# Kernel tuning notes

Hardware: AMD Instinct MI355X
Metric: run time of the kernel (lower is better)

## Reference

```python
import jax, jax.numpy as jnp
import numpy as np

B, T, K, H = 8, 1024, 512, 8
MASKED = True

def setup_inputs() -> dict:
    key = jax.random.key(0)
    ks = jax.random.split(key, 6)
    s = 0.02
    return {
        "x": jax.random.normal(ks[0], (B, T, K), dtype=jnp.float32),
        "Wq": jax.random.normal(ks[1], (K, H * K), dtype=jnp.float32) * s,
        "Wk": jax.random.normal(ks[2], (K, H * K), dtype=jnp.float32) * s,
        "Wv": jax.random.normal(ks[3], (K, H * K), dtype=jnp.float32) * s,
        "Wu": jax.random.normal(ks[4], (H * K, K), dtype=jnp.float32) * s,
        "bu": jnp.zeros((K,), dtype=jnp.float32),
    }

def reference(x, Wq, Wk, Wv, Wu, bu):
    b, t, k = x.shape
    h = H
    scale = k ** (-0.25)  # applied to both q and k, as in the torch module
    q = (x @ Wq).reshape(b, t, h, k) * scale
    kk = (x @ Wk).reshape(b, t, h, k) * scale
    v = (x @ Wv).reshape(b, t, h, k)
    # scores: [b, h, t_q, t_k]
    dot = jnp.einsum("bthk,bshk->bhts", q, kk)
    if MASKED:
        causal = jnp.tril(jnp.ones((t, t), dtype=bool))
        dot = jnp.where(causal, dot, -jnp.inf)
    attn = jax.nn.softmax(dot, axis=-1)
    out = jnp.einsum("bhts,bshk->bthk", attn, v).reshape(b, t, h * k)
    return out @ Wu + bu
```

## Files before the change

kernel.cpp:

```cpp
#include <hip/hip_runtime.h>
#include <hip/hip_bf16.h>

#define T_SEQ 1024
#define NH 8
#define DH 512
#define HK 4096

typedef __attribute__((ext_vector_type(8))) __bf16 bf16x8;
typedef __attribute__((ext_vector_type(4))) float f32x4;

#define QK_SCALE 0.21022410381342863f
#define QK_SCALE_LOG2E 0.30328926584f

static __device__ __forceinline__ unsigned short f2bu(float f) {
  union { __hip_bfloat16 h; unsigned short u; } cv;
  cv.h = __float2bfloat16(f);
  return cv.u;
}

#define GLOAD_LDS16(gsrc, ldst) \
  __builtin_amdgcn_global_load_lds((const __attribute__((address_space(1))) void*)(gsrc), \
                                   (__attribute__((address_space(3))) void*)(ldst), 16, 0, 0)

__global__ void cvt_bf16_kernel(const float* __restrict__ in, unsigned short* __restrict__ out, int n4) {
  int i = blockIdx.x * blockDim.x + threadIdx.x;
  if (i >= n4) return;
  const float4 v = reinterpret_cast<const float4*>(in)[i];
  ushort4 u; u.x = f2bu(v.x); u.y = f2bu(v.y); u.z = f2bu(v.z); u.w = f2bu(v.w);
  reinterpret_cast<ushort4*>(out)[i] = u;
}

__global__ void transpose_cvt_kernel(const float* __restrict__ in, unsigned short* __restrict__ out,
                                     int R, int C) {
  __shared__ float tile[32][33];
  const int c0 = blockIdx.x * 32, r0 = blockIdx.y * 32;
  const int tx = threadIdx.x, ty = threadIdx.y;
  #pragma unroll
  for (int i = ty; i < 32; i += 8)
    tile[i][tx] = in[(size_t)(r0 + i) * C + (c0 + tx)];
  __syncthreads();
  #pragma unroll
  for (int i = ty; i < 32; i += 8)
    out[(size_t)(c0 + i) * R + (r0 + tx)] = f2bu(tile[tx][i]);
}

__global__ void transpose_cvt3_kernel(const float* __restrict__ Wq, const float* __restrict__ Wk,
                                      const float* __restrict__ Wv, unsigned short* __restrict__ out) {
  __shared__ float tile[32][33];
  const float* in = (blockIdx.z == 0) ? Wq : (blockIdx.z == 1) ? Wk : Wv;
  unsigned short* dst = out + (size_t)blockIdx.z * 4096 * 512;
  const int c0 = blockIdx.x * 32, r0 = blockIdx.y * 32;
  const int tx = threadIdx.x, ty = threadIdx.y;
  #pragma unroll
  for (int i = ty; i < 32; i += 8)
    tile[i][tx] = in[(size_t)(r0 + i) * 4096 + (c0 + tx)];
  __syncthreads();
  #pragma unroll
  for (int i = ty; i < 32; i += 8)
    dst[(size_t)(c0 + i) * 512 + (r0 + tx)] = f2bu(tile[tx][i]);
}

__global__ __launch_bounds__(256, 4)
void gemm_qkv(const unsigned short* __restrict__ A,
              const unsigned short* __restrict__ B,
              unsigned short* __restrict__ Qo,
              unsigned short* __restrict__ Ko,
              unsigned short* __restrict__ Vo) {
  __shared__ __align__(16) char smem[32768];
  char* As = smem;
  char* Bs = smem + 16384;
  const int tid = threadIdx.x, lane = tid & 63, w = tid >> 6;
  const int wr = w >> 1, wc = w & 1;
  const int bid = blockIdx.x;
  const int x = bid & 7, inner = bid >> 3;
  const int p0 = (x * 12 + inner % 12) * 128;
  const int p1 = (inner / 12) * 128;
  const int Kd = 512;

  f32x4 acc[4][4];
  #pragma unroll
  for (int i = 0; i < 4; ++i)
    #pragma unroll
    for (int j = 0; j < 4; ++j)
      acc[i][j] = f32x4{0.f, 0.f, 0.f, 0.f};

  for (int kt = 0; kt < Kd; kt += 64) {
    __syncthreads();
    #pragma unroll
    for (int is = 0; is < 4; ++is) {
      const int ob = is * 4096 + w * 1024;
      const int ol = ob + lane * 16;
      const int row = ol >> 7;
      const int bo = ol & 127;
      const int sw = (row & 7) << 4;
      GLOAD_LDS16((const char*)A + ((size_t)(p0 + row) * Kd + kt) * 2 + (bo ^ sw), As + ob);
      GLOAD_LDS16((const char*)B + ((size_t)(p1 + row) * Kd + kt) * 2 + (bo ^ sw), Bs + ob);
    }
    __syncthreads();
    #pragma unroll
    for (int ks = 0; ks < 2; ++ks) {
      bf16x8 af[4], bfr[4];
      #pragma unroll
      for (int mi = 0; mi < 4; ++mi) {
        const int row = wr * 64 + mi * 16 + (lane & 15);
        af[mi] = *reinterpret_cast<const bf16x8*>(
            As + row * 128 + ((ks * 64 + ((lane >> 4) << 4)) ^ ((row & 7) << 4)));
      }
      #pragma unroll
      for (int ni = 0; ni < 4; ++ni) {
        const int row = wc * 64 + ni * 16 + (lane & 15);
        bfr[ni] = *reinterpret_cast<const bf16x8*>(
            Bs + row * 128 + ((ks * 64 + ((lane >> 4) << 4)) ^ ((row & 7) << 4)));
      }
      #pragma unroll
      for (int mi = 0; mi < 4; ++mi)
        #pragma unroll
        for (int ni = 0; ni < 4; ++ni)
          acc[mi][ni] = __builtin_amdgcn_mfma_f32_16x16x32_bf16(af[mi], bfr[ni], acc[mi][ni], 0, 0, 0);
    }
  }

  const int region = p0 >> 12;
  if (region < 2) {
    const float qs = (region == 0) ? QK_SCALE_LOG2E : QK_SCALE;
    unsigned short* dst = (region == 0) ? Qo : Ko;
    #pragma unroll
    for (int mi = 0; mi < 4; ++mi) {
      #pragma unroll
      for (int ni = 0; ni < 4; ++ni) {
        const int n = p0 + wr * 64 + mi * 16 + ((lane >> 4) << 2);
        const int m = p1 + wc * 64 + ni * 16 + (lane & 15);
        const int b = m >> 10, t = m & 1023;
        const int nr = n & 4095, h = nr >> 9, d = nr & 511;
        ushort4 u;
        u.x = f2bu(acc[mi][ni][0] * qs); u.y = f2bu(acc[mi][ni][1] * qs);
        u.z = f2bu(acc[mi][ni][2] * qs); u.w = f2bu(acc[mi][ni][3] * qs);
        *reinterpret_cast<ushort4*>(&dst[((size_t)((b * NH + h) * T_SEQ + t)) * DH + d]) = u;
      }
    }
  } else {
    __syncthreads();
    unsigned short* Vl = reinterpret_cast<unsigned short*>(smem);
    const int key = (lane >> 4) << 3;
    #pragma unroll
    for (int mi = 0; mi < 4; ++mi) {
      #pragma unroll
      for (int ni = 0; ni < 4; ++ni) {
        const int dl = wr * 64 + mi * 16 + ((lane >> 4) << 2);
        const int tl = wc * 64 + ni * 16 + (lane & 15);
        #pragma unroll
        for (int r = 0; r < 4; ++r)
          Vl[(dl + r) * 128 + (tl ^ key)] = f2bu(acc[mi][ni][r]);
      }
    }
    __syncthreads();
    const int bb = p1 >> 10, t0 = p1 & 1023;
    const int hh = (p0 - 8192) >> 9, d0 = p0 & 511;
    unsigned short* vdst = Vo + ((size_t)(bb * NH + hh) * DH + d0) * T_SEQ + t0;
    #pragma unroll
    for (int i = 0; i < 8; ++i) {
      const int idx = i * 256 + tid;
      const int dr = idx >> 4, tc = (idx & 15) * 8;
      const int key2 = ((dr >> 2) & 3) << 3;
      *reinterpret_cast<uint4*>(vdst + (size_t)dr * T_SEQ + tc) =
          *reinterpret_cast<const uint4*>(Vl + dr * 128 + (tc ^ key2));
    }
  }
}

__global__ __launch_bounds__(256, 4)
void gemm_out(const unsigned short* __restrict__ A,
              const unsigned short* __restrict__ B,
              const float* __restrict__ bias,
              float* __restrict__ C) {
  __shared__ __align__(16) char As[8192];
  __shared__ __align__(16) char Bs[16384];
  const int tid = threadIdx.x, lane = tid & 63, w = tid >> 6;
  const int bid = blockIdx.x;
  const int x = bid & 7, inner = bid >> 3;
  const int mtiles_per_xcd = gridDim.x >> 7;
  const int c0 = (inner & 15) * 32;
  const int m0 = (x * mtiles_per_xcd + (inner >> 4)) * 64;
  const int Kd = HK;

  f32x4 acc[2];
  acc[0] = f32x4{0.f, 0.f, 0.f, 0.f};
  acc[1] = f32x4{0.f, 0.f, 0.f, 0.f};

  for (int kt = 0; kt < Kd; kt += 128) {
    __syncthreads();
    #pragma unroll
    for (int is = 0; is < 2; ++is) {
      const int ob = is * 4096 + w * 1024;
      const int ol = ob + lane * 16;
      const int row = ol >> 8, bo = ol & 255;
      GLOAD_LDS16((const char*)A + ((size_t)(c0 + row) * Kd + kt) * 2 + (bo ^ ((row & 15) << 4)), As + ob);
    }
    #pragma unroll
    for (int is = 0; is < 4; ++is) {
      const int ob = is * 4096 + w * 1024;
      const int ol = ob + lane * 16;
      const int row = ol >> 8, bo = ol & 255;
      GLOAD_LDS16((const char*)B + ((size_t)(m0 + row) * Kd + kt) * 2 + (bo ^ ((row & 15) << 4)), Bs + ob);
    }
    __syncthreads();
    #pragma unroll
    for (int ks = 0; ks < 4; ++ks) {
      const int ko = ks * 64 + ((lane >> 4) << 4);
      bf16x8 af0, af1, bf;
      { const int row = (lane & 15);
        af0 = *reinterpret_cast<const bf16x8*>(As + row * 256 + (ko ^ ((row & 15) << 4))); }
      { const int row = 16 + (lane & 15);
        af1 = *reinterpret_cast<const bf16x8*>(As + row * 256 + (ko ^ ((row & 15) << 4))); }
      { const int row = w * 16 + (lane & 15);
        bf = *reinterpret_cast<const bf16x8*>(Bs + row * 256 + (ko ^ ((row & 15) << 4))); }
      acc[0] = __builtin_amdgcn_mfma_f32_16x16x32_bf16(af0, bf, acc[0], 0, 0, 0);
      acc[1] = __builtin_amdgcn_mfma_f32_16x16x32_bf16(af1, bf, acc[1], 0, 0, 0);
    }
  }

  const int m = m0 + w * 16 + (lane & 15);
  #pragma unroll
  for (int fc = 0; fc < 2; ++fc) {
    const int c = c0 + fc * 16 + ((lane >> 4) << 2);
    const float4 bn = *reinterpret_cast<const float4*>(&bias[c]);
    float4 v;
    v.x = acc[fc][0] + bn.x; v.y = acc[fc][1] + bn.y;
    v.z = acc[fc][2] + bn.z; v.w = acc[fc][3] + bn.w;
    *reinterpret_cast<float4*>(&C[(size_t)m * DH + c]) = v;
  }
}

__global__ __launch_bounds__(512, 1)
void attn_kernel(const unsigned short* __restrict__ Qg,
                 const unsigned short* __restrict__ Kg,
                 const unsigned short* __restrict__ Vtg,
                 unsigned short* __restrict__ Og) {
  __shared__ __align__(16) char Ks[2][32768];
  __shared__ __align__(16) char Vts[2][32768];
  __shared__ float S_lds[64 * 32];
  __shared__ __align__(16) char P_lds[64 * 64];
  __shared__ float Mrow[64], Lrow[64], Arow[64];
  __shared__ int rflag;

  const int tid = threadIdx.x, lane = tid & 63, w = tid >> 6;
  const int n = blockIdx.x;
  const int h = n & 7, p = (n >> 3) & 7, b = n >> 6;
  const int bh = b * NH + h;

  const unsigned short* Qbase = Qg + (size_t)bh * T_SEQ * DH;
  const char* Kbase = (const char*)(Kg + (size_t)bh * T_SEQ * DH);
  const char* Vbase = (const char*)(Vtg + (size_t)bh * DH * T_SEQ);

  auto stage = [&](int st, int buf) {
    #pragma unroll
    for (int is = 0; is < 4; ++is) {
      const int ob = is * 8192 + w * 1024;
      const int ol = ob + lane * 16;
      { const int row = ol >> 10, bo = ol & 1023;
        GLOAD_LDS16(Kbase + (size_t)(st * 32 + row) * 1024 + (bo ^ ((row & 7) << 4)), Ks[buf] + ob); }
      { const int row = ol >> 6, bo = ol & 63;
        GLOAD_LDS16(Vbase + (size_t)row * 2048 + st * 64 + (bo ^ ((row & 3) << 4)), Vts[buf] + ob); }
    }
  };

  for (int rep = 0; rep < 2; ++rep) {
    const int qt = rep ? 15 - p : p;
    const int nst = 2 * qt + 2;
    __syncthreads();

    bf16x8 qreg[16];
    {
      const int qrow = qt * 64 + ((w >> 1) << 4) + (lane & 15);
      const unsigned short* qp = Qbase + (size_t)qrow * DH + ((lane >> 4) << 3);
      #pragma unroll
      for (int k2 = 0; k2 < 16; ++k2)
        qreg[k2] = *reinterpret_cast<const bf16x8*>(qp + k2 * 32);
    }

    f32x4 o[2][8];
    #pragma unroll
    for (int mi = 0; mi < 2; ++mi)
      #pragma unroll
      for (int ni = 0; ni < 8; ++ni)
        o[mi][ni] = f32x4{0.f, 0.f, 0.f, 0.f};

    if (tid < 64) { Mrow[tid] = -INFINITY; Lrow[tid] = 0.f; }

    int cur = 0;
    stage(0, 0);

    for (int st = 0; st < nst; ++st) {
      __syncthreads();
      if (st + 1 < nst) stage(st + 1, cur ^ 1);
      if (tid == 0) rflag = 0;

      {
        const int krow = ((w & 1) << 4) + (lane & 15);
        const char* kr = Ks[cur] + krow * 1024;
        const int sw = (krow & 7) << 4;
        f32x4 sA = f32x4{0.f, 0.f, 0.f, 0.f};
        f32x4 sB = f32x4{0.f, 0.f, 0.f, 0.f};
        __builtin_amdgcn_s_setprio(1);
        #pragma unroll
        for (int ks = 0; ks < 16; ks += 2) {
          bf16x8 kf0 = *reinterpret_cast<const bf16x8*>(kr + ((ks * 64 + ((lane >> 4) << 4)) ^ sw));
          bf16x8 kf1 = *reinterpret_cast<const bf16x8*>(kr + (((ks + 1) * 64 + ((lane >> 4) << 4)) ^ sw));
          sA = __builtin_amdgcn_mfma_f32_16x16x32_bf16(qreg[ks], kf0, sA, 0, 0, 0);
          sB = __builtin_amdgcn_mfma_f32_16x16x32_bf16(qreg[ks + 1], kf1, sB, 0, 0, 0);
        }
        __builtin_amdgcn_s_setprio(0);
        const f32x4 s = sA + sB;
        const int col = ((w & 1) << 4) + (lane & 15);
        const int rbase = ((w >> 1) << 4) + ((lane >> 4) << 2);
        #pragma unroll
        for (int r = 0; r < 4; ++r)
          S_lds[(rbase + r) * 32 + (col ^ (((rbase + r) & 7) << 2))] = s[r];
      }
      asm volatile("s_waitcnt lgkmcnt(0)" ::: "memory");
      __builtin_amdgcn_sched_barrier(0);
      __builtin_amdgcn_s_barrier();

      {
        const int r = tid >> 3, cg = tid & 7;
        const int grow = qt * 64 + r;
        const int base = r * 32 + ((cg * 4) ^ ((r & 7) << 2));
        float sv[4];
        #pragma unroll
        for (int j = 0; j < 4; ++j) {
          const int c = cg * 4 + j;
          const float x = S_lds[base + j];
          sv[j] = (st * 32 + c > grow) ? -INFINITY : x;
        }
        float pm = fmaxf(fmaxf(sv[0], sv[1]), fmaxf(sv[2], sv[3]));
        pm = fmaxf(pm, __shfl_xor(pm, 1));
        pm = fmaxf(pm, __shfl_xor(pm, 2));
        pm = fmaxf(pm, __shfl_xor(pm, 4));
        const float m_old = Mrow[r];
        const bool defer = (pm <= m_old + 11.0f);
        const float m_new = defer ? m_old : pm;
        float ps;
        ushort4 pu;
        { float p0 = exp2f(sv[0] - m_new), p1 = exp2f(sv[1] - m_new),
                p2 = exp2f(sv[2] - m_new), p3 = exp2f(sv[3] - m_new);
          ps = p0 + p1 + p2 + p3;
          pu.x = f2bu(p0); pu.y = f2bu(p1); pu.z = f2bu(p2); pu.w = f2bu(p3); }
        *reinterpret_cast<ushort4*>(P_lds + r * 64 + ((cg * 8) ^ ((r & 3) << 4))) = pu;
        ps += __shfl_xor(ps, 1);
        ps += __shfl_xor(ps, 2);
        ps += __shfl_xor(ps, 4);
        if (cg == 0) {
          const float alpha = defer ? 1.0f : exp2f(m_old - m_new);
          if (!defer) { rflag = 1; Mrow[r] = m_new; }
          Arow[r] = alpha;
          Lrow[r] = alpha * Lrow[r] + ps;
        }
      }
      asm volatile("s_waitcnt lgkmcnt(0)" ::: "memory");
      __builtin_amdgcn_sched_barrier(0);
      __builtin_amdgcn_s_barrier();

      {
        bf16x8 pf[2];
        #pragma unroll
        for (int mi = 0; mi < 2; ++mi) {
          const int pr = ((w >> 2) << 5) + mi * 16 + (lane & 15);
          pf[mi] = *reinterpret_cast<const bf16x8*>(
              P_lds + pr * 64 + ((((lane >> 4) << 4)) ^ ((pr & 3) << 4)));
        }
        if (rflag) {
          #pragma unroll
          for (int mi = 0; mi < 2; ++mi) {
            const int rb = ((w >> 2) << 5) + mi * 16 + ((lane >> 4) << 2);
            const f32x4 al = f32x4{Arow[rb], Arow[rb + 1], Arow[rb + 2], Arow[rb + 3]};
            #pragma unroll
            for (int ni = 0; ni < 8; ++ni) o[mi][ni] *= al;
          }
        }
        __builtin_amdgcn_s_setprio(1);
        #pragma unroll
        for (int ni = 0; ni < 8; ++ni) {
          const int vr = ((w & 3) << 7) + ni * 16 + (lane & 15);
          bf16x8 vf = *reinterpret_cast<const bf16x8*>(
              Vts[cur] + vr * 64 + ((((lane >> 4) << 4)) ^ ((vr & 3) << 4)));
          o[0][ni] = __builtin_amdgcn_mfma_f32_16x16x32_bf16(pf[0], vf, o[0][ni], 0, 0, 0);
          o[1][ni] = __builtin_amdgcn_mfma_f32_16x16x32_bf16(pf[1], vf, o[1][ni], 0, 0, 0);
        }
        __builtin_amdgcn_s_setprio(0);
      }
      cur ^= 1;
    }

    #pragma unroll
    for (int mi = 0; mi < 2; ++mi) {
      const int rb = ((w >> 2) << 5) + mi * 16 + ((lane >> 4) << 2);
      f32x4 li;
      #pragma unroll
      for (int r = 0; r < 4; ++r) li[r] = 1.f / Lrow[rb + r];
      #pragma unroll
      for (int ni = 0; ni < 8; ++ni) {
        const int d = ((w & 3) << 7) + ni * 16 + (lane & 15);
        const size_t base = ((size_t)(b * T_SEQ + qt * 64 + rb) * NH + h) * DH + d;
        #pragma unroll
        for (int r = 0; r < 4; ++r)
          Og[base + (size_t)r * NH * DH] = f2bu(o[mi][ni][r] * li[r]);
      }
    }
  }
}

extern "C" void kernel_launch(void* const* d_in, const int* in_sizes, int n_in,
                              void* d_out, int out_size, void* d_ws, size_t ws_size,
                              hipStream_t stream) {
  (void)in_sizes; (void)n_in; (void)out_size;
  const float* x  = (const float*)d_in[0];
  const float* Wq = (const float*)d_in[1];
  const float* Wk = (const float*)d_in[2];
  const float* Wv = (const float*)d_in[3];
  const float* Wu = (const float*)d_in[4];
  const float* bu = (const float*)d_in[5];
  float* out = (float*)d_out;

  const size_t PERS = (size_t)8192 * 512 * 2 + 3 * (size_t)4096 * 512 * 2 + (size_t)512 * 4096 * 2;
  int NB = 8;
  while (NB > 1 && PERS + 4 * ((size_t)NB * 1024 * 4096 * 2) + 65536 > ws_size) NB >>= 1;

  size_t off = 0;
  auto wsp = [&](size_t bytes) {
    char* p = (char*)d_ws + off;
    off += (bytes + 255) & ~(size_t)255;
    return p;
  };
  unsigned short* xb   = (unsigned short*)wsp((size_t)8192 * 512 * 2);
  unsigned short* Wcat = (unsigned short*)wsp(3 * (size_t)4096 * 512 * 2);
  unsigned short* Wut  = (unsigned short*)wsp((size_t)512 * 4096 * 2);
  const size_t CHB = (size_t)NB * 1024 * 4096 * 2;
  unsigned short* Qc = (unsigned short*)wsp(CHB);
  unsigned short* Kc = (unsigned short*)wsp(CHB);
  unsigned short* Vc = (unsigned short*)wsp(CHB);
  unsigned short* Oc = (unsigned short*)wsp(CHB);

  cvt_bf16_kernel<<<4096, 256, 0, stream>>>(x, xb, 8192 * 512 / 4);
  transpose_cvt3_kernel<<<dim3(128, 16, 3), dim3(32, 8), 0, stream>>>(Wq, Wk, Wv, Wcat);
  transpose_cvt_kernel<<<dim3(16, 128), dim3(32, 8), 0, stream>>>(Wu, Wut, 4096, 512);

  const int nchunks = 8 / NB;
  for (int c = 0; c < nchunks; ++c) {
    const unsigned short* xc = xb + (size_t)c * NB * 1024 * 512;
    gemm_qkv<<<96 * NB * 8, 256, 0, stream>>>(Wcat, xc, Qc, Kc, Vc);
    attn_kernel<<<64 * NB, 512, 0, stream>>>(Qc, Kc, Vc, Oc);
    gemm_out<<<256 * NB, 256, 0, stream>>>(Wut, Oc, bu, out + (size_t)c * NB * 1024 * 512);
  }
}
```

Before: 421.9 us.

## Enlarge QKV GEMM tile to 256x256 with double-buffered LDS pipeline

The QKV projection GEMM moves from 128x128 tiles with 4 waves to 256x256 tiles with 8 waves. It also double-buffers the K=128-wide LDS stages so global-to-LDS loads overlap the MFMA compute, using explicit vmcnt waits and barriers. The goal is more data reuse per tile and hidden load latency. In exchange it uses 128KB of LDS at one block per CU, a much smaller grid, and a reworked V-transpose epilogue.

```diff
diff --git a/kernel.cpp b/kernel.cpp
--- a/kernel.cpp
+++ b/kernel.cpp
@@ -60,63 +60,82 @@
     dst[(size_t)(c0 + i) * 512 + (r0 + tx)] = f2bu(tile[tx][i]);
 }
 
-__global__ __launch_bounds__(256, 4)
+__global__ __launch_bounds__(512, 1)
 void gemm_qkv(const unsigned short* __restrict__ A,
               const unsigned short* __restrict__ B,
               unsigned short* __restrict__ Qo,
               unsigned short* __restrict__ Ko,
               unsigned short* __restrict__ Vo) {
-  __shared__ __align__(16) char smem[32768];
-  char* As = smem;
-  char* Bs = smem + 16384;
+  __shared__ __align__(16) char smem[131072];
   const int tid = threadIdx.x, lane = tid & 63, w = tid >> 6;
-  const int wr = w >> 1, wc = w & 1;
+  const int wm = w >> 2, wn = w & 3;
   const int bid = blockIdx.x;
   const int x = bid & 7, inner = bid >> 3;
-  const int p0 = (x * 12 + inner % 12) * 128;
-  const int p1 = (inner / 12) * 128;
-  const int Kd = 512;
-
-  f32x4 acc[4][4];
-  #pragma unroll
-  for (int i = 0; i < 4; ++i)
+  const int p0 = (x * 6 + inner % 6) * 256;
+  const int p1 = (inner / 6) * 256;
+
+  f32x4 acc[8][4];
+  #pragma unroll
+  for (int i = 0; i < 8; ++i)
     #pragma unroll
     for (int j = 0; j < 4; ++j)
       acc[i][j] = f32x4{0.f, 0.f, 0.f, 0.f};
 
-  for (int kt = 0; kt < Kd; kt += 64) {
-    __syncthreads();
+  auto stage = [&](int t, int c) {
+    const int kt = t * 128;
     #pragma unroll
     for (int is = 0; is < 4; ++is) {
-      const int ob = is * 4096 + w * 1024;
+      const int ob = is * 8192 + w * 1024;
       const int ol = ob + lane * 16;
-      const int row = ol >> 7;
-      const int bo = ol & 127;
+      const int row = ol >> 7, bo = ol & 127;
       const int sw = (row & 7) << 4;
-      GLOAD_LDS16((const char*)A + ((size_t)(p0 + row) * Kd + kt) * 2 + (bo ^ sw), As + ob);
-      GLOAD_LDS16((const char*)B + ((size_t)(p1 + row) * Kd + kt) * 2 + (bo ^ sw), Bs + ob);
-    }
-    __syncthreads();
+      GLOAD_LDS16((const char*)A + (size_t)(p0 + row) * 1024 + kt + (bo ^ sw),
+                  smem + c * 32768 + ob);
+      GLOAD_LDS16((const char*)B + (size_t)(p1 + row) * 1024 + kt + (bo ^ sw),
+                  smem + 65536 + c * 32768 + ob);
+    }
+  };
+
+  stage(0, 0);
+  stage(1, 1);
+  asm volatile("s_waitcnt vmcnt(8)" ::: "memory");
+  __builtin_amdgcn_sched_barrier(0);
+  __builtin_amdgcn_s_barrier();
+
+  for (int t = 0; t < 8; ++t) {
+    const int c = t & 1;
+    const char* Ab = smem + c * 32768;
+    const char* Bb = smem + 65536 + c * 32768;
     #pragma unroll
     for (int ks = 0; ks < 2; ++ks) {
-      bf16x8 af[4], bfr[4];
-      #pragma unroll
-      for (int mi = 0; mi < 4; ++mi) {
-        const int row = wr * 64 + mi * 16 + (lane & 15);
+      bf16x8 af[8], bf[4];
+      #pragma unroll
+      for (int mi = 0; mi < 8; ++mi) {
+        const int row = wm * 128 + mi * 16 + (lane & 15);
         af[mi] = *reinterpret_cast<const bf16x8*>(
-            As + row * 128 + ((ks * 64 + ((lane >> 4) << 4)) ^ ((row & 7) << 4)));
+            Ab + row * 128 + ((ks * 64 + ((lane >> 4) << 4)) ^ ((row & 7) << 4)));
       }
       #pragma unroll
       for (int ni = 0; ni < 4; ++ni) {
-        const int row = wc * 64 + ni * 16 + (lane & 15);
-        bfr[ni] = *reinterpret_cast<const bf16x8*>(
-            Bs + row * 128 + ((ks * 64 + ((lane >> 4) << 4)) ^ ((row & 7) << 4)));
-      }
-      #pragma unroll
-      for (int mi = 0; mi < 4; ++mi)
+        const int row = wn * 64 + ni * 16 + (lane & 15);
+        bf[ni] = *reinterpret_cast<const bf16x8*>(
+            Bb + row * 128 + ((ks * 64 + ((lane >> 4) << 4)) ^ ((row & 7) << 4)));
+      }
+      #pragma unroll
+      for (int mi = 0; mi < 8; ++mi)
         #pragma unroll
         for (int ni = 0; ni < 4; ++ni)
-          acc[mi][ni] = __builtin_amdgcn_mfma_f32_16x16x32_bf16(af[mi], bfr[ni], acc[mi][ni], 0, 0, 0);
+          acc[mi][ni] = __builtin_amdgcn_mfma_f32_16x16x32_bf16(af[mi], bf[ni], acc[mi][ni], 0, 0, 0);
+    }
+    asm volatile("" ::: "memory");
+    __builtin_amdgcn_sched_barrier(0);
+    __builtin_amdgcn_s_barrier();
+    if (t + 2 < 8) stage(t + 2, c);
+    if (t + 1 < 8) {
+      if (t + 2 < 8) asm volatile("s_waitcnt vmcnt(8)" ::: "memory");
+      else           asm volatile("s_waitcnt vmcnt(0)" ::: "memory");
+      __builtin_amdgcn_sched_barrier(0);
+      __builtin_amdgcn_s_barrier();
     }
   }
 
@@ -125,11 +144,11 @@
     const float qs = (region == 0) ? QK_SCALE_LOG2E : QK_SCALE;
     unsigned short* dst = (region == 0) ? Qo : Ko;
     #pragma unroll
-    for (int mi = 0; mi < 4; ++mi) {
+    for (int mi = 0; mi < 8; ++mi) {
       #pragma unroll
       for (int ni = 0; ni < 4; ++ni) {
-        const int n = p0 + wr * 64 + mi * 16 + ((lane >> 4) << 2);
-        const int m = p1 + wc * 64 + ni * 16 + (lane & 15);
+        const int n = p0 + wm * 128 + mi * 16 + ((lane >> 4) << 2);
+        const int m = p1 + wn * 64 + ni * 16 + (lane & 15);
         const int b = m >> 10, t = m & 1023;
         const int nr = n & 4095, h = nr >> 9, d = nr & 511;
         ushort4 u;
@@ -139,31 +158,32 @@
       }
     }
   } else {
-    __syncthreads();
+    __builtin_amdgcn_sched_barrier(0);
+    __builtin_amdgcn_s_barrier();
     unsigned short* Vl = reinterpret_cast<unsigned short*>(smem);
-    const int key = (lane >> 4) << 3;
-    #pragma unroll
-    for (int mi = 0; mi < 4; ++mi) {
+    #pragma unroll
+    for (int mi = 0; mi < 8; ++mi) {
       #pragma unroll
       for (int ni = 0; ni < 4; ++ni) {
-        const int dl = wr * 64 + mi * 16 + ((lane >> 4) << 2);
-        const int tl = wc * 64 + ni * 16 + (lane & 15);
-        #pragma unroll
-        for (int r = 0; r < 4; ++r)
-          Vl[(dl + r) * 128 + (tl ^ key)] = f2bu(acc[mi][ni][r]);
+        const int dl0 = wm * 128 + mi * 16 + ((lane >> 4) << 2);
+        const int tl = wn * 64 + ni * 16 + (lane & 15);
+        #pragma unroll
+        for (int r = 0; r < 4; ++r) {
+          const int dl = dl0 + r;
+          Vl[dl * 256 + (tl ^ ((dl & 7) << 3))] = f2bu(acc[mi][ni][r]);
+        }
       }
     }
     __syncthreads();
     const int bb = p1 >> 10, t0 = p1 & 1023;
-    const int hh = (p0 - 8192) >> 9, d0 = p0 & 511;
+    const int hh = (p0 - 8192) >> 9, d0 = (p0 - 8192) & 511;
     unsigned short* vdst = Vo + ((size_t)(bb * NH + hh) * DH + d0) * T_SEQ + t0;
     #pragma unroll
-    for (int i = 0; i < 8; ++i) {
-      const int idx = i * 256 + tid;
-      const int dr = idx >> 4, tc = (idx & 15) * 8;
-      const int key2 = ((dr >> 2) & 3) << 3;
+    for (int i = 0; i < 16; ++i) {
+      const int idx = i * 512 + tid;
+      const int dr = idx >> 5, tc = (idx & 31) * 8;
       *reinterpret_cast<uint4*>(vdst + (size_t)dr * T_SEQ + tc) =
-          *reinterpret_cast<const uint4*>(Vl + dr * 128 + (tc ^ key2));
+          *reinterpret_cast<const uint4*>(Vl + dr * 256 + (tc ^ ((dr & 7) << 3)));
     }
   }
 }
@@ -447,7 +467,7 @@
   const int nchunks = 8 / NB;
   for (int c = 0; c < nchunks; ++c) {
     const unsigned short* xc = xb + (size_t)c * NB * 1024 * 512;
-    gemm_qkv<<<96 * NB * 8, 256, 0, stream>>>(Wcat, xc, Qc, Kc, Vc);
+    gemm_qkv<<<192 * NB, 512, 0, stream>>>(Wcat, xc, Qc, Kc, Vc);
     attn_kernel<<<64 * NB, 512, 0, stream>>>(Qc, Kc, Vc, Oc);
     gemm_out<<<256 * NB, 256, 0, stream>>>(Wut, Oc, bu, out + (size_t)c * NB * 1024 * 512);
   }
```

Result: faster. 405.4 us (-3.9%).
